# Performance work log

Hardware: AMD Instinct MI355X
Metric: run time of the kernel (lower is better)

Reference implementation:

```python
import jax, jax.numpy as jnp
import numpy as np
from jax import lax

RF, NLF, MESH, FUSION = 64, 16, 16, 64


def _conv3x3(x, w, b):
    # stride 1, pad 1, ksize 3 == SAME
    y = lax.conv_general_dilated(x, w, (1, 1), 'SAME',
                                 dimension_numbers=('NCHW', 'OIHW', 'NCHW'))
    return y + b[None, :, None, None]


def _bn(x, g, b, m, v, eps=1e-5):
    scale = g / jnp.sqrt(v + eps)
    return (x - m[None, :, None, None]) * scale[None, :, None, None] + b[None, :, None, None]


def _rct_block(x, w1, b1, g, be, m, v, w2, b2):
    # extra_conv=True: Conv -> BN -> SiLU -> Conv (all stride 1)
    h = jax.nn.silu(_bn(_conv3x3(x, w1, b1), g, be, m, v))
    return _conv3x3(h, w2, b2)


def setup_inputs():
    key = jax.random.key(0)
    ks = jax.random.split(key, 8)
    B, H, W = 4, 512, 512
    return {
        'feature': jax.random.normal(ks[0], (B, RF, H, W), jnp.float32),
        'p_low': jax.random.normal(ks[1], (B, FUSION, MESH + 1, MESH + 1), jnp.float32),
        'r_w1': jax.random.normal(ks[2], (FUSION, FUSION, 3, 3), jnp.float32) * 0.05,
        'r_b1': jnp.zeros((FUSION,), jnp.float32),
        'r_gamma': jnp.ones((FUSION,), jnp.float32),
        'r_beta': jnp.zeros((FUSION,), jnp.float32),
        'r_mean': jnp.zeros((FUSION,), jnp.float32),
        'r_var': jnp.ones((FUSION,), jnp.float32),
        'r_w2': jax.random.normal(ks[3], (RF * NLF, FUSION, 3, 3), jnp.float32) * 0.05,
        'r_b2': jnp.zeros((RF * NLF,), jnp.float32),
        't_w1': jax.random.normal(ks[4], (FUSION, FUSION, 3, 3), jnp.float32) * 0.05,
        't_b1': jnp.zeros((FUSION,), jnp.float32),
        't_gamma': jnp.ones((FUSION,), jnp.float32),
        't_beta': jnp.zeros((FUSION,), jnp.float32),
        't_mean': jnp.zeros((FUSION,), jnp.float32),
        't_var': jnp.ones((FUSION,), jnp.float32),
        't_w2': jax.random.normal(ks[5], (3 * NLF, FUSION, 3, 3), jnp.float32) * 0.05,
        't_b2': jnp.zeros((3 * NLF,), jnp.float32),
    }


def reference(feature, p_low, r_w1, r_b1, r_gamma, r_beta, r_mean, r_var, r_w2, r_b2,
              t_w1, t_b1, t_gamma, t_beta, t_mean, t_var, t_w2, t_b2):
    B, C, H, W = feature.shape
    M = MESH
    mh, mw = H // M, W // M  # H,W divisible by mesh_size -> pad_tensor is identity
    P = mh * mw

    r_l = _rct_block(p_low, r_w1, r_b1, r_gamma, r_beta, r_mean, r_var, r_w2, r_b2)  # [B, RF*NLF, M+1, M+1]
    t_l = _rct_block(p_low, t_w1, t_b1, t_gamma, t_beta, t_mean, t_var, t_w2, t_b2)  # [B, 3*NLF, M+1, M+1]

    # channel dim factors as (feat, nlf); corners concat along nlf axis in order
    # (i,j), (i,j+1), (i+1,j), (i+1,j+1) -> K = 4*NLF keys per tile
    rc = r_l.reshape(B, RF, NLF, M + 1, M + 1)
    rk = jnp.concatenate([rc[..., :M, :M], rc[..., :M, 1:],
                          rc[..., 1:, :M], rc[..., 1:, 1:]], axis=2)  # [B,RF,4NLF,M,M]
    tc = t_l.reshape(B, 3, NLF, M + 1, M + 1)
    tk = jnp.concatenate([tc[..., :M, :M], tc[..., :M, 1:],
                          tc[..., 1:, :M], tc[..., 1:, 1:]], axis=2)  # [B,3,4NLF,M,M]

    # split feature into tiles: [B, M, M, P, RF] (row-major pixel order within tile)
    f = feature.reshape(B, RF, M, mh, M, mw).transpose(0, 2, 4, 3, 5, 1).reshape(B, M, M, P, RF)

    scale = 1.0 / jnp.sqrt(jnp.float32(RF))
    att = jnp.einsum('bxypr,brkxy->bxypk', f, rk) * scale  # [B,M,M,P,4NLF]
    att = jax.nn.softmax(att, axis=-1)
    out = jnp.einsum('bxypk,bckxy->bxycp', att, tk)  # [B,M,M,3,P]

    Y = out.reshape(B, M, M, 3, mh, mw).transpose(0, 3, 1, 4, 2, 5).reshape(B, 3, H, W)
    return Y
```

## Files before the change

kernel.cpp:

```cpp
#include <hip/hip_runtime.h>

typedef unsigned short u16;
typedef __bf16 bf16x8 __attribute__((ext_vector_type(8)));
typedef unsigned short us8 __attribute__((ext_vector_type(8)));
typedef float f32x4 __attribute__((ext_vector_type(4)));
typedef unsigned int u32x4 __attribute__((ext_vector_type(4)));

union U8u { us8 s; u16 u[8]; };

__device__ __forceinline__ u16 f2bf(float f){
  unsigned u = __builtin_bit_cast(unsigned, f);
  u += 0x7fffu + ((u >> 16) & 1u);
  return (u16)(u >> 16);
}
__device__ __forceinline__ bf16x8 asbf(us8 x){ return __builtin_bit_cast(bf16x8, x); }

#define MFMA16(a,b,c) __builtin_amdgcn_mfma_f32_16x16x32_bf16((a),(b),(c),0,0,0)

__device__ __forceinline__ void stage_zero2(u16* sS, int tid){
  uint* z = (uint*)sS;
  for (int i = tid; i < 12996; i += 256) z[i] = 0u;
}

__device__ __forceinline__ void stage_src_f32T(const float* __restrict__ src,
                                               u16* sS, int tid){
  for (int i4 = tid; i4 < 4624; i4 += 256){
    int e = i4 * 4;
    f32x4 dv = *(const f32x4*)(src + e);
    #pragma unroll
    for (int t = 0; t < 4; t++){
      int ee = e + t;
      int ci = ee / 289; int rr = ee - ci*289;
      int oy = rr / 17;  int ox = rr - oy*17;
      sS[((oy+1)*19 + ox+1)*72 + ci] = f2bf(dv[t]);
    }
  }
}

__device__ __forceinline__ void stage_src_bf16T(const u16* __restrict__ src,
                                                u16* sS, int tid){
  for (int i8 = tid; i8 < 2312; i8 += 256){
    int e = i8 * 8;
    U8u dv; dv.s = *(const us8*)(src + e);
    #pragma unroll
    for (int t = 0; t < 8; t++){
      int ee = e + t;
      int ci = ee / 289; int rr = ee - ci*289;
      int oy = rr / 17;  int ox = rr - oy*17;
      sS[((oy+1)*19 + ox+1)*72 + ci] = dv.u[t];
    }
  }
}

__device__ __forceinline__ void stage_w_f32(const float* __restrict__ w, int m0,
                                            u16* sW, int tid){
  for (int i4 = tid; i4 < 2304; i4 += 256){
    int e = i4 * 4;
    int co = e / 576; int r0 = e - co*576;
    f32x4 wv = *(const f32x4*)(w + (size_t)(m0+co)*576 + r0);
    #pragma unroll
    for (int t = 0; t < 4; t++){
      int r = r0 + t; int cin = r / 9; int tap = r - cin*9;
      sW[co*584 + tap*64 + cin] = f2bf(wv[t]);
    }
  }
}

__device__ __forceinline__ f32x4 conv_tile2(const u16* sS, const u16* sW,
                                            int nt, int l15, int q)
{
  int p = nt*16 + l15; int pc = p > 288 ? 288 : p;
  int oy = pc / 17, ox = pc - oy*17;
  f32x4 acc = {0.f, 0.f, 0.f, 0.f};
  #pragma unroll
  for (int ks = 0; ks < 18; ks++){
    const int tap = ks >> 1;
    const int dy = tap / 3, dx = tap - dy*3;
    int pix2 = (oy+dy)*19 + (ox+dx);
    us8 bv = *(const us8*)(sS + pix2*72 + (ks & 1)*32 + q*8);
    us8 av = *(const us8*)(sW + l15*584 + ks*32 + q*8);
    acc = MFMA16(asbf(av), asbf(bv), acc);
  }
  return acc;
}

__global__ __launch_bounds__(256) void conv1_k(
    const float* __restrict__ p_low,
    const float* __restrict__ wR, const float* __restrict__ b1R,
    const float* __restrict__ gR, const float* __restrict__ beR,
    const float* __restrict__ mR, const float* __restrict__ vR,
    const float* __restrict__ wT, const float* __restrict__ b1T,
    const float* __restrict__ gT, const float* __restrict__ beT,
    const float* __restrict__ mT, const float* __restrict__ vT,
    u16* __restrict__ hR, u16* __restrict__ hT)
{
  __shared__ __attribute__((aligned(16))) u16 sS[25992];
  __shared__ __attribute__((aligned(16))) u16 sW[9344];
  int tid = threadIdx.x;
  int bx = blockIdx.x;
  int job = bx >> 6;
  int b = (bx >> 4) & 3;
  int m0 = ((bx >> 2) & 3) << 4;
  int px = bx & 3;
  int nt0 = px * 5, ntEnd = nt0 + 5 > 19 ? 19 : nt0 + 5;
  const float* w  = job ? wT  : wR;
  const float* b1 = job ? b1T : b1R;
  const float* g  = job ? gT  : gR;
  const float* be = job ? beT : beR;
  const float* mn = job ? mT  : mR;
  const float* vr = job ? vT  : vR;
  u16* out = job ? hT : hR;
  const float* src = p_low + (size_t)b * 18496;

  stage_zero2(sS, tid);
  __syncthreads();
  stage_src_f32T(src, sS, tid);
  stage_w_f32(w, m0, sW, tid);
  __syncthreads();

  int lane = tid & 63, wave = tid >> 6;
  int l15 = lane & 15, q = lane >> 4;
  float scl[4], sft[4];
  #pragma unroll
  for (int e = 0; e < 4; e++){
    int co = m0 + q*4 + e;
    float s = g[co] / sqrtf(vr[co] + 1e-5f);
    scl[e] = s;
    sft[e] = (b1[co] - mn[co]) * s + be[co];
  }
  for (int nt = nt0 + wave; nt < ntEnd; nt += 4){
    f32x4 acc = conv_tile2(sS, sW, nt, l15, q);
    int p = nt*16 + l15;
    if (p < 289){
      #pragma unroll
      for (int e = 0; e < 4; e++){
        float y = acc[e]*scl[e] + sft[e];
        float si = y / (1.f + __expf(-y));
        out[(size_t)(b*64 + m0 + q*4 + e)*289 + p] = f2bf(si);
      }
    }
  }
}

__global__ __launch_bounds__(256) void conv2_k(
    const u16* __restrict__ hR, const u16* __restrict__ hT,
    const float* __restrict__ w2R, const float* __restrict__ b2R,
    const float* __restrict__ w2T, const float* __restrict__ b2T,
    u16* __restrict__ rlq, float* __restrict__ tlq)
{
  __shared__ __attribute__((aligned(16))) u16 sS[25992];
  __shared__ __attribute__((aligned(16))) u16 sW[9344];
  int tid = threadIdx.x;
  int bx = blockIdx.x;
  const float *w, *bias; const u16* src;
  int b, m0, px, isR;
  if (bx < 512){
    isR = 1; b = bx >> 7; int rem = bx & 127;
    m0 = (rem >> 1) << 4; px = rem & 1;
    src = hR + (size_t)b*18496; w = w2R; bias = b2R;
  } else {
    isR = 0; int i = bx - 512; b = i / 6; int rr = i - b*6;
    m0 = (rr >> 1) << 4; px = rr & 1;
    src = hT + (size_t)b*18496; w = w2T; bias = b2T;
  }
  int nt0 = px * 10, ntEnd = px ? 19 : 10;

  stage_zero2(sS, tid);
  __syncthreads();
  stage_src_bf16T(src, sS, tid);
  stage_w_f32(w, m0, sW, tid);
  __syncthreads();

  int lane = tid & 63, wave = tid >> 6;
  int l15 = lane & 15, q = lane >> 4;
  float bs[4];
  #pragma unroll
  for (int e = 0; e < 4; e++) bs[e] = bias[m0 + q*4 + e];
  const float PSC = 0.18033688f;
  for (int nt = nt0 + wave; nt < ntEnd; nt += 4){
    f32x4 acc = conv_tile2(sS, sW, nt, l15, q);
    int p = nt*16 + l15;
    if (p < 289){
      if (isR){
        uint2 pk;
        pk.x = (uint)f2bf((acc[0]+bs[0])*PSC)
             | ((uint)f2bf((acc[1]+bs[1])*PSC) << 16);
        pk.y = (uint)f2bf((acc[2]+bs[2])*PSC)
             | ((uint)f2bf((acc[3]+bs[3])*PSC) << 16);
        *(uint2*)(rlq + ((size_t)b*289 + p)*1024 + m0 + q*4) = pk;
      } else {
        f32x4 ov = {acc[0]+bs[0], acc[1]+bs[1], acc[2]+bs[2], acc[3]+bs[3]};
        *(f32x4*)(tlq + ((size_t)b*289 + p)*48 + m0 + q*4) = ov;
      }
    }
  }
}

__global__ __launch_bounds__(256) void attn_k(
    const uint* __restrict__ feat,
    const u16* __restrict__ rlq, const float* __restrict__ tlq,
    float* __restrict__ out)
{
  __shared__ __attribute__((aligned(16))) u16 rkT[4608];
  __shared__ __attribute__((aligned(16))) float tkF[256];
  int tid = threadIdx.x;
  int ty = blockIdx.x, tx = blockIdx.y, b = blockIdx.z;
  int lane = tid & 63, wave = tid >> 6;
  int l15 = lane & 15, q = lane >> 4;

  {
    int corner = wave;
    int pix = (tx + (corner >> 1))*17 + ty + (corner & 1);
    const u16* sp = rlq + ((size_t)b*289 + pix)*1024 + lane*16;
    U8u v0, v1; v0.s = *(const us8*)sp; v1.s = *(const us8*)(sp + 8);
    #pragma unroll
    for (int nl = 0; nl < 8; nl++){
      rkT[(corner*16 + nl)*72 + lane]     = v0.u[nl];
      rkT[(corner*16 + 8 + nl)*72 + lane] = v1.u[nl];
    }
  }
  if (tid < 192){
    int corner = tid / 48; int idx = tid - corner*48;
    int pix = (tx + (corner >> 1))*17 + ty + (corner & 1);
    int c = idx >> 4, nl = idx & 15;
    tkF[c*64 + corner*16 + nl] = tlq[((size_t)b*289 + pix)*48 + idx];
  } else {
    tkF[192 + (tid - 192)] = 1.f;
  }
  __syncthreads();

  bf16x8 frk[4][2];
  #pragma unroll
  for (int nt = 0; nt < 4; nt++)
    #pragma unroll
    for (int ks = 0; ks < 2; ks++)
      frk[nt][ks] = __builtin_bit_cast(bf16x8,
          *(const us8*)(rkT + (nt*16 + l15)*72 + ks*32 + q*8));

  f32x4 tkc[3][4];
  #pragma unroll
  for (int c = 0; c < 3; c++)
    #pragma unroll
    for (int nt = 0; nt < 4; nt++)
      tkc[c][nt] = *(const f32x4*)(tkF + c*64 + nt*16 + q*4);

  const size_t HW = (size_t)512*512;
  for (int cnk = 0; cnk < 16; cnk++){
    int irow = (wave << 3) + (cnk >> 1);
    int j0 = (cnk & 1) << 4;
    int hh = tx*32 + irow;
    const uint* fb = feat + ((size_t)b*64 + q*8)*HW + (size_t)hh*512
                          + (ty*32 + j0 + l15);
    uint r0[8], r1[8];
    #pragma unroll
    for (int j = 0; j < 8; j++){
      r0[j] = fb[(size_t)j*HW];
      r1[j] = fb[(size_t)(j+32)*HW];
    }
    u32x4 p0, p1;
    #pragma unroll
    for (int j2 = 0; j2 < 4; j2++){
      p0[j2] = __builtin_amdgcn_perm(r0[2*j2+1], r0[2*j2], 0x07060302u);
      p1[j2] = __builtin_amdgcn_perm(r1[2*j2+1], r1[2*j2], 0x07060302u);
    }
    bf16x8 A0 = __builtin_bit_cast(bf16x8, p0);
    bf16x8 A1 = __builtin_bit_cast(bf16x8, p1);

    f32x4 acc[4];
    #pragma unroll
    for (int nt = 0; nt < 4; nt++){
      f32x4 zz = {0.f, 0.f, 0.f, 0.f};
      zz = MFMA16(frk[nt][0], A0, zz);
      zz = MFMA16(frk[nt][1], A1, zz);
      acc[nt] = zz;
    }
    float den = 0.f, o0 = 0.f, o1 = 0.f, o2 = 0.f;
    #pragma unroll
    for (int nt = 0; nt < 4; nt++)
      #pragma unroll
      for (int e = 0; e < 4; e++){
        float p = __builtin_amdgcn_exp2f(acc[nt][e]);
        den += p;
        o0 = fmaf(p, tkc[0][nt][e], o0);
        o1 = fmaf(p, tkc[1][nt][e], o1);
        o2 = fmaf(p, tkc[2][nt][e], o2);
      }
    o0  += __shfl_xor(o0, 16, 64);
    o1  += __shfl_xor(o1, 16, 64);
    o2  += __shfl_xor(o2, 16, 64);
    den += __shfl_xor(den, 16, 64);
    o0  += __shfl_xor(o0, 32, 64);
    o1  += __shfl_xor(o1, 32, 64);
    o2  += __shfl_xor(o2, 32, 64);
    den += __shfl_xor(den, 32, 64);
    float rin = __builtin_amdgcn_rcpf(den);
    float val = (q == 0) ? o0 : ((q == 1) ? o1 : o2);
    if (q < 3)
      out[((size_t)(b*3 + q)*512 + hh)*512 + (ty*32 + j0 + l15)] = val * rin;
  }
}

extern "C" void kernel_launch(void* const* d_in, const int* in_sizes, int n_in,
                              void* d_out, int out_size, void* d_ws, size_t ws_size,
                              hipStream_t stream)
{
  (void)in_sizes; (void)n_in; (void)out_size; (void)ws_size;
  const uint*  feature = (const uint*)d_in[0];
  const float* p_low = (const float*)d_in[1];
  const float* r_w1 = (const float*)d_in[2];
  const float* r_b1 = (const float*)d_in[3];
  const float* r_g  = (const float*)d_in[4];
  const float* r_be = (const float*)d_in[5];
  const float* r_m  = (const float*)d_in[6];
  const float* r_v  = (const float*)d_in[7];
  const float* r_w2 = (const float*)d_in[8];
  const float* r_b2 = (const float*)d_in[9];
  const float* t_w1 = (const float*)d_in[10];
  const float* t_b1 = (const float*)d_in[11];
  const float* t_g  = (const float*)d_in[12];
  const float* t_be = (const float*)d_in[13];
  const float* t_m  = (const float*)d_in[14];
  const float* t_v  = (const float*)d_in[15];
  const float* t_w2 = (const float*)d_in[16];
  const float* t_b2 = (const float*)d_in[17];

  char* ws = (char*)d_ws;
  u16* hR = (u16*)ws;
  u16* hT = hR + (size_t)4*64*289;
  u16* rlq = (u16*)(ws + 295936);
  float* tlq = (float*)(ws + 295936 + 2367488);
  float* outp = (float*)d_out;

  hipLaunchKernelGGL(conv1_k, dim3(128), dim3(256), 0, stream,
      p_low, r_w1, r_b1, r_g, r_be, r_m, r_v,
      t_w1, t_b1, t_g, t_be, t_m, t_v, hR, hT);
  hipLaunchKernelGGL(conv2_k, dim3(536), dim3(256), 0, stream,
      hR, hT, r_w2, r_b2, t_w2, t_b2, rlq, tlq);
  hipLaunchKernelGGL(attn_k, dim3(16, 16, 4), dim3(256), 0, stream,
      feature, rlq, tlq, outp);
}
```

Baseline: 456.9 us.

## Prefetch feature rows in attention, pixel-major intermediates, fewer conv blocks

The attention kernel now loads the next chunk's feature values while the current chunk runs its MFMAs. It also raises wave priority around the MFMA block and packs the softmax accumulation into two-wide FMAs. The conv1 output changes to pixel-major layout, so conv2 can stage its input with vector copies instead of scattered 16-bit transposes. The conv kernels drop their pixel split, leaving each block to cover all 19 tiles, which roughly halves conv2's block count and quarters conv1's. The trade-off is fewer blocks in the conv stages and higher register pressure from the prefetch buffers in attention.

Result: faster. 445.1 us (-2.6%).

```diff
diff --git a/kernel.cpp b/kernel.cpp
--- a/kernel.cpp
+++ b/kernel.cpp
@@ -4,6 +4,7 @@
 typedef __bf16 bf16x8 __attribute__((ext_vector_type(8)));
 typedef unsigned short us8 __attribute__((ext_vector_type(8)));
 typedef float f32x4 __attribute__((ext_vector_type(4)));
+typedef float f32x2 __attribute__((ext_vector_type(2)));
 typedef unsigned int u32x4 __attribute__((ext_vector_type(4)));
 
 union U8u { us8 s; u16 u[8]; };
@@ -37,18 +38,13 @@
   }
 }
 
-__device__ __forceinline__ void stage_src_bf16T(const u16* __restrict__ src,
-                                                u16* sS, int tid){
+__device__ __forceinline__ void stage_src_pm(const u16* __restrict__ src,
+                                             u16* sS, int tid){
   for (int i8 = tid; i8 < 2312; i8 += 256){
-    int e = i8 * 8;
-    U8u dv; dv.s = *(const us8*)(src + e);
-    #pragma unroll
-    for (int t = 0; t < 8; t++){
-      int ee = e + t;
-      int ci = ee / 289; int rr = ee - ci*289;
-      int oy = rr / 17;  int ox = rr - oy*17;
-      sS[((oy+1)*19 + ox+1)*72 + ci] = dv.u[t];
-    }
+    int pix = i8 >> 3, c0 = (i8 & 7) << 3;
+    us8 v = *(const us8*)(src + ((size_t)pix << 6) + c0);
+    int oy = pix / 17, ox = pix - oy*17;
+    *(us8*)(sS + ((oy+1)*19 + ox+1)*72 + c0) = v;
   }
 }
 
@@ -98,11 +94,9 @@
   __shared__ __attribute__((aligned(16))) u16 sW[9344];
   int tid = threadIdx.x;
   int bx = blockIdx.x;
-  int job = bx >> 6;
-  int b = (bx >> 4) & 3;
-  int m0 = ((bx >> 2) & 3) << 4;
-  int px = bx & 3;
-  int nt0 = px * 5, ntEnd = nt0 + 5 > 19 ? 19 : nt0 + 5;
+  int job = bx >> 4;
+  int b = (bx >> 2) & 3;
+  int m0 = (bx & 3) << 4;
   const float* w  = job ? wT  : wR;
   const float* b1 = job ? b1T : b1R;
   const float* g  = job ? gT  : gR;
@@ -128,16 +122,20 @@
     scl[e] = s;
     sft[e] = (b1[co] - mn[co]) * s + be[co];
   }
-  for (int nt = nt0 + wave; nt < ntEnd; nt += 4){
+  for (int nt = wave; nt < 19; nt += 4){
     f32x4 acc = conv_tile2(sS, sW, nt, l15, q);
     int p = nt*16 + l15;
     if (p < 289){
+      float si[4];
       #pragma unroll
       for (int e = 0; e < 4; e++){
         float y = acc[e]*scl[e] + sft[e];
-        float si = y / (1.f + __expf(-y));
-        out[(size_t)(b*64 + m0 + q*4 + e)*289 + p] = f2bf(si);
+        si[e] = y / (1.f + __expf(-y));
       }
+      uint2 pk;
+      pk.x = (uint)f2bf(si[0]) | ((uint)f2bf(si[1]) << 16);
+      pk.y = (uint)f2bf(si[2]) | ((uint)f2bf(si[3]) << 16);
+      *(uint2*)(out + ((size_t)b*289 + p)*64 + m0 + q*4) = pk;
     }
   }
 }
@@ -153,21 +151,18 @@
   int tid = threadIdx.x;
   int bx = blockIdx.x;
   const float *w, *bias; const u16* src;
-  int b, m0, px, isR;
-  if (bx < 512){
-    isR = 1; b = bx >> 7; int rem = bx & 127;
-    m0 = (rem >> 1) << 4; px = rem & 1;
+  int b, m0, isR;
+  if (bx < 256){
+    isR = 1; b = bx >> 6; m0 = (bx & 63) << 4;
     src = hR + (size_t)b*18496; w = w2R; bias = b2R;
   } else {
-    isR = 0; int i = bx - 512; b = i / 6; int rr = i - b*6;
-    m0 = (rr >> 1) << 4; px = rr & 1;
+    isR = 0; int i = bx - 256; b = i / 3; m0 = (i - b*3) << 4;
     src = hT + (size_t)b*18496; w = w2T; bias = b2T;
   }
-  int nt0 = px * 10, ntEnd = px ? 19 : 10;
 
   stage_zero2(sS, tid);
   __syncthreads();
-  stage_src_bf16T(src, sS, tid);
+  stage_src_pm(src, sS, tid);
   stage_w_f32(w, m0, sW, tid);
   __syncthreads();
 
@@ -177,7 +172,7 @@
   #pragma unroll
   for (int e = 0; e < 4; e++) bs[e] = bias[m0 + q*4 + e];
   const float PSC = 0.18033688f;
-  for (int nt = nt0 + wave; nt < ntEnd; nt += 4){
+  for (int nt = wave; nt < 19; nt += 4){
     f32x4 acc = conv_tile2(sS, sW, nt, l15, q);
     int p = nt*16 + l15;
     if (p < 289){
@@ -224,8 +219,6 @@
     int pix = (tx + (corner >> 1))*17 + ty + (corner & 1);
     int c = idx >> 4, nl = idx & 15;
     tkF[c*64 + corner*16 + nl] = tlq[((size_t)b*289 + pix)*48 + idx];
-  } else {
-    tkF[192 + (tid - 192)] = 1.f;
   }
   __syncthreads();
 
@@ -244,29 +237,41 @@
     for (int nt = 0; nt < 4; nt++)
       tkc[c][nt] = *(const f32x4*)(tkF + c*64 + nt*16 + q*4);
 
-  const size_t HW = (size_t)512*512;
+  const uint HW = 512u*512u;
+  const uint* fpb = feat + (size_t)b*64*HW;
+  uint offbase = (uint)(q*8)*HW + (uint)(tx*32 + wave*8)*512u
+               + (uint)(ty*32 + l15);
+
+  uint r0[8], r1[8];
+  #pragma unroll
+  for (int j = 0; j < 8; j++){
+    r0[j] = fpb[offbase + (uint)j*HW];
+    r1[j] = fpb[offbase + (uint)(j+32)*HW];
+  }
+
+  #pragma unroll
   for (int cnk = 0; cnk < 16; cnk++){
-    int irow = (wave << 3) + (cnk >> 1);
-    int j0 = (cnk & 1) << 4;
-    int hh = tx*32 + irow;
-    const uint* fb = feat + ((size_t)b*64 + q*8)*HW + (size_t)hh*512
-                          + (ty*32 + j0 + l15);
-    uint r0[8], r1[8];
-    #pragma unroll
-    for (int j = 0; j < 8; j++){
-      r0[j] = fb[(size_t)j*HW];
-      r1[j] = fb[(size_t)(j+32)*HW];
-    }
-    u32x4 p0, p1;
+    u32x4 p0v, p1v;
     #pragma unroll
     for (int j2 = 0; j2 < 4; j2++){
-      p0[j2] = __builtin_amdgcn_perm(r0[2*j2+1], r0[2*j2], 0x07060302u);
-      p1[j2] = __builtin_amdgcn_perm(r1[2*j2+1], r1[2*j2], 0x07060302u);
-    }
-    bf16x8 A0 = __builtin_bit_cast(bf16x8, p0);
-    bf16x8 A1 = __builtin_bit_cast(bf16x8, p1);
+      p0v[j2] = __builtin_amdgcn_perm(r0[2*j2+1], r0[2*j2], 0x07060302u);
+      p1v[j2] = __builtin_amdgcn_perm(r1[2*j2+1], r1[2*j2], 0x07060302u);
+    }
+    bf16x8 A0 = __builtin_bit_cast(bf16x8, p0v);
+    bf16x8 A1 = __builtin_bit_cast(bf16x8, p1v);
+
+    if (cnk < 15){
+      int nc = cnk + 1;
+      uint noff = offbase + (uint)((nc >> 1)*512 + ((nc & 1) << 4));
+      #pragma unroll
+      for (int j = 0; j < 8; j++){
+        r0[j] = fpb[noff + (uint)j*HW];
+        r1[j] = fpb[noff + (uint)(j+32)*HW];
+      }
+    }
 
     f32x4 acc[4];
+    __builtin_amdgcn_s_setprio(1);
     #pragma unroll
     for (int nt = 0; nt < 4; nt++){
       f32x4 zz = {0.f, 0.f, 0.f, 0.f};
@@ -274,17 +279,34 @@
       zz = MFMA16(frk[nt][1], A1, zz);
       acc[nt] = zz;
     }
-    float den = 0.f, o0 = 0.f, o1 = 0.f, o2 = 0.f;
-    #pragma unroll
-    for (int nt = 0; nt < 4; nt++)
-      #pragma unroll
-      for (int e = 0; e < 4; e++){
-        float p = __builtin_amdgcn_exp2f(acc[nt][e]);
-        den += p;
-        o0 = fmaf(p, tkc[0][nt][e], o0);
-        o1 = fmaf(p, tkc[1][nt][e], o1);
-        o2 = fmaf(p, tkc[2][nt][e], o2);
-      }
+    __builtin_amdgcn_s_setprio(0);
+
+    f32x2 den2 = {0.f,0.f}, o0v = {0.f,0.f}, o1v = {0.f,0.f}, o2v = {0.f,0.f};
+    #pragma unroll
+    for (int nt = 0; nt < 4; nt++){
+      f32x2 pa, pb;
+      pa[0] = __builtin_amdgcn_exp2f(acc[nt][0]);
+      pa[1] = __builtin_amdgcn_exp2f(acc[nt][1]);
+      pb[0] = __builtin_amdgcn_exp2f(acc[nt][2]);
+      pb[1] = __builtin_amdgcn_exp2f(acc[nt][3]);
+      den2 += pa; den2 += pb;
+      f32x2 t0a = {tkc[0][nt][0], tkc[0][nt][1]};
+      f32x2 t0b = {tkc[0][nt][2], tkc[0][nt][3]};
+      f32x2 t1a = {tkc[1][nt][0], tkc[1][nt][1]};
+      f32x2 t1b = {tkc[1][nt][2], tkc[1][nt][3]};
+      f32x2 t2a = {tkc[2][nt][0], tkc[2][nt][1]};
+      f32x2 t2b = {tkc[2][nt][2], tkc[2][nt][3]};
+      o0v = __builtin_elementwise_fma(pa, t0a, o0v);
+      o0v = __builtin_elementwise_fma(pb, t0b, o0v);
+      o1v = __builtin_elementwise_fma(pa, t1a, o1v);
+      o1v = __builtin_elementwise_fma(pb, t1b, o1v);
+      o2v = __builtin_elementwise_fma(pa, t2a, o2v);
+      o2v = __builtin_elementwise_fma(pb, t2b, o2v);
+    }
+    float den = den2[0] + den2[1];
+    float o0 = o0v[0] + o0v[1];
+    float o1 = o1v[0] + o1v[1];
+    float o2 = o2v[0] + o2v[1];
     o0  += __shfl_xor(o0, 16, 64);
     o1  += __shfl_xor(o1, 16, 64);
     o2  += __shfl_xor(o2, 16, 64);
@@ -295,6 +317,8 @@
     den += __shfl_xor(den, 32, 64);
     float rin = __builtin_amdgcn_rcpf(den);
     float val = (q == 0) ? o0 : ((q == 1) ? o1 : o2);
+    int hh = tx*32 + wave*8 + (cnk >> 1);
+    int j0 = (cnk & 1) << 4;
     if (q < 3)
       out[((size_t)(b*3 + q)*512 + hh)*512 + (ty*32 + j0 + l15)] = val * rin;
   }
@@ -326,15 +350,15 @@
 
   char* ws = (char*)d_ws;
   u16* hR = (u16*)ws;
-  u16* hT = hR + (size_t)4*64*289;
+  u16* hT = hR + (size_t)4*289*64;
   u16* rlq = (u16*)(ws + 295936);
   float* tlq = (float*)(ws + 295936 + 2367488);
   float* outp = (float*)d_out;
 
-  hipLaunchKernelGGL(conv1_k, dim3(128), dim3(256), 0, stream,
+  hipLaunchKernelGGL(conv1_k, dim3(32), dim3(256), 0, stream,
       p_low, r_w1, r_b1, r_g, r_be, r_m, r_v,
       t_w1, t_b1, t_g, t_be, t_m, t_v, hR, hT);
-  hipLaunchKernelGGL(conv2_k, dim3(536), dim3(256), 0, stream,
+  hipLaunchKernelGGL(conv2_k, dim3(268), dim3(256), 0, stream,
       hR, hT, r_w2, r_b2, t_w2, t_b2, rlq, tlq);
   hipLaunchKernelGGL(attn_k, dim3(16, 16, 4), dim3(256), 0, stream,
       feature, rlq, tlq, outp);
```
